# Kernel optimization log

Hardware: AMD Instinct MI355X
Metric: run time of the kernel (lower is better)

The kernel has to match this reference:

```python
import jax, jax.numpy as jnp
import numpy as np

NUM_TAGS = 48
START = 46
STOP = 47
B = 1024
S = 512
NEG_INF = -10000.0


def setup_inputs() -> dict:
    key = jax.random.key(0)
    k1, k2, k3, k4 = jax.random.split(key, 4)
    emissions = jax.random.normal(k1, (B, S, NUM_TAGS), dtype=jnp.float32)
    tags = jax.random.randint(k2, (B, S), 0, 46, dtype=jnp.int32)
    lengths = jax.random.randint(k3, (B,), S // 2, S + 1, dtype=jnp.int32)
    mask = (jnp.arange(S, dtype=jnp.int32)[None, :] < lengths[:, None]).astype(jnp.int32)
    # transitions parameter: uniform(-0.1, 0.1), then constraints from reset_parameters
    transitions = jax.random.uniform(k4, (NUM_TAGS, NUM_TAGS), dtype=jnp.float32,
                                     minval=-0.1, maxval=0.1)
    transitions = transitions.at[:, START].set(NEG_INF).at[STOP, :].set(NEG_INF)
    return {"emissions": emissions, "tags": tags, "mask": mask, "transitions": transitions}


def _log_sum_exp(x, axis):
    # matches torch helper: max + log(clamp(sum(exp(x - max)), 1e-10))
    m = jnp.max(x, axis=axis, keepdims=True)
    s = jnp.sum(jnp.exp(x - m), axis=axis, keepdims=True)
    return jnp.squeeze(m + jnp.log(jnp.clip(s, 1e-10)), axis=axis)


def _forward_alg(emissions, transitions, mask):
    b, s, t = emissions.shape
    alpha0 = jnp.full((b, t), NEG_INF, dtype=emissions.dtype).at[:, START].set(0.0)

    def step(alpha, xs):
        emit, m = xs  # emit: (B, T), m: (B,)
        # (B, prev, next)
        nxt = alpha[:, :, None] + transitions[None, :, :] + emit[:, None, :]
        alpha_t = _log_sum_exp(nxt, axis=1)
        alpha = jnp.where(m[:, None] > 0, alpha_t, alpha)
        return alpha, None

    alpha, _ = jax.lax.scan(step, alpha0,
                            (jnp.transpose(emissions, (1, 0, 2)), mask.T))
    terminal = alpha + transitions[STOP][None, :]
    return _log_sum_exp(terminal, axis=1)  # (B,)


def _score_sequence(emissions, transitions, tags, mask):
    b, s, _ = emissions.shape
    start_col = jnp.full((b, 1), START, dtype=tags.dtype)
    tws = jnp.concatenate([start_col, tags], axis=1)  # (B, S+1)
    # transitions[next, prev] per the original _score_sequence
    trans_sc = transitions[tws[:, 1:], tws[:, :-1]]  # (B, S)
    emit_sc = jnp.take_along_axis(emissions, tags[:, :, None].astype(jnp.int32), axis=2)[..., 0]
    score = jnp.sum((trans_sc + emit_sc) * mask.astype(emissions.dtype), axis=1)
    lengths = jnp.sum(mask, axis=1)
    last_tags = jnp.take_along_axis(tags, (lengths - 1)[:, None], axis=1)[:, 0]
    return score + transitions[STOP, last_tags]


def reference(emissions, tags, mask, transitions):
    log_z = _forward_alg(emissions, transitions, mask)
    gold = _score_sequence(emissions, transitions, tags, mask)
    return jnp.mean(log_z - gold)
```

## Files before the change

kernel.cpp:

```cpp
#include <hip/hip_runtime.h>
#include <hip/hip_bf16.h>
#include <stdint.h>
#include <math.h>

#define SLEN 512
#define NT 48
#define TAG_START 46
#define TAG_STOP 47

typedef __attribute__((ext_vector_type(8))) short bf16x8;
typedef __attribute__((ext_vector_type(4))) float f32x4;

typedef const uint32_t __attribute__((address_space(1)))* gptr_t;
typedef uint32_t __attribute__((address_space(3)))* lptr_t;

__device__ __forceinline__ float bcastf(float v, int l) {
  return __int_as_float(__builtin_amdgcn_readlane(__float_as_int(v), l));
}
__device__ __forceinline__ void gload16(const float* g, float* l) {
  __builtin_amdgcn_global_load_lds((gptr_t)(uintptr_t)g, (lptr_t)(uintptr_t)l,
                                   16, 0, 0);
}
__device__ __forceinline__ uint32_t pk2(float a, float b) {
  float2 f;
  f.x = a;
  f.y = b;
  __hip_bfloat162 bb = __float22bfloat162_rn(f);
  uint32_t u;
  __builtin_memcpy(&u, &bb, 4);
  return u;
}

__global__ __launch_bounds__(64, 1) void crf_fwd_kernel(
    const float* __restrict__ em, const int* __restrict__ tags,
    const int* __restrict__ mask, const float* __restrict__ Tr,
    float* __restrict__ ws) {
  const int b = blockIdx.x;
  const int lane = threadIdx.x;
  const int g = lane >> 4;
  const int n = lane & 15;
  __shared__ __align__(16) float fb[2][32 * NT];
  __shared__ __align__(16) float bbuf[2][32 * NT];

  const int* mrow = mask + (size_t)b * SLEN;
  int lc = 0;
  for (int t = lane; t < SLEN; t += 64) lc += mrow[t];
#pragma unroll
  for (int d = 32; d >= 1; d >>= 1) lc += __shfl_xor(lc, d);
  const int len = lc;

  bf16x8 Af[3][2], Ab[3][2];
#pragma unroll
  for (int t = 0; t < 3; ++t) {
#pragma unroll
    for (int c = 0; c < 2; ++c) {
      union { uint32_t u[4]; bf16x8 v; } tf, tb;
#pragma unroll
      for (int ep = 0; ep < 4; ++ep) {
        float ff[2], fbk[2];
#pragma unroll
        for (int h = 0; h < 2; ++h) {
          const int e = 2 * ep + h;
          const int kl = (e < 4) ? (4 * g + e) : (16 + 4 * g + (e - 4));
          const int ig = 32 * c + kl;
          ff[h] = (ig < NT) ? __expf(Tr[ig * NT + 16 * t + n]) : 0.0f;
          fbk[h] = (ig < NT) ? __expf(Tr[(16 * t + n) * NT + ig]) : 0.0f;
        }
        tf.u[ep] = pk2(ff[0], ff[1]);
        tb.u[ep] = pk2(fbk[0], fbk[1]);
      }
      Af[t][c] = tf.v;
      Ab[t][c] = tb.v;
    }
  }

  f32x4 vf0 = {0.f, 0.f, 0.f, 0.f}, vf1 = vf0, vf2 = vf0;
  if (lane == 48) vf2.z = 1.0f;
  f32x4 vb0 = vf0, vb1 = vf0, vb2 = vf0;
  if (n == 0) {
    const f32x4 one4 = {1.f, 1.f, 1.f, 1.f};
    vb0 = one4;
    vb1 = one4;
    vb2 = one4;
  }
  int cbits = 0;

  const float* embase = em + (size_t)b * SLEN * NT;
  const f32x4 z4 = {0.f, 0.f, 0.f, 0.f};

  auto pairstep = [&](const float* xfp, const float* xbp) {
    const f32x4 xf0 = *(const f32x4*)(xfp + 4 * g);
    const f32x4 xf1 = *(const f32x4*)(xfp + 16 + 4 * g);
    const f32x4 xf2 = *(const f32x4*)(xfp + 32 + 4 * g);
    const f32x4 xb0 = *(const f32x4*)(xbp + 4 * g);
    const f32x4 xb1 = *(const f32x4*)(xbp + 16 + 4 * g);
    const f32x4 xb2 = *(const f32x4*)(xbp + 32 + 4 * g);
    union { uint32_t u[4]; bf16x8 v; } F0, F1;
    F0.u[0] = pk2(vf0.x, vf0.y);
    F0.u[1] = pk2(vf0.z, vf0.w);
    F0.u[2] = pk2(vf1.x, vf1.y);
    F0.u[3] = pk2(vf1.z, vf1.w);
    F1.u[0] = pk2(vf2.x, vf2.y);
    F1.u[1] = pk2(vf2.z, vf2.w);
    F1.u[2] = 0u;
    F1.u[3] = 0u;
    f32x4 af0 = __builtin_amdgcn_mfma_f32_16x16x32_bf16(Af[0][0], F0.v, z4, 0, 0, 0);
    f32x4 af1 = __builtin_amdgcn_mfma_f32_16x16x32_bf16(Af[1][0], F0.v, z4, 0, 0, 0);
    f32x4 af2 = __builtin_amdgcn_mfma_f32_16x16x32_bf16(Af[2][0], F0.v, z4, 0, 0, 0);
    af0 = __builtin_amdgcn_mfma_f32_16x16x32_bf16(Af[0][1], F1.v, af0, 0, 0, 0);
    af1 = __builtin_amdgcn_mfma_f32_16x16x32_bf16(Af[1][1], F1.v, af1, 0, 0, 0);
    af2 = __builtin_amdgcn_mfma_f32_16x16x32_bf16(Af[2][1], F1.v, af2, 0, 0, 0);
    const f32x4 y0 = vb0 * xb0, y1 = vb1 * xb1, y2 = vb2 * xb2;
    union { uint32_t u[4]; bf16x8 v; } G0, G1;
    G0.u[0] = pk2(y0.x, y0.y);
    G0.u[1] = pk2(y0.z, y0.w);
    G0.u[2] = pk2(y1.x, y1.y);
    G0.u[3] = pk2(y1.z, y1.w);
    G1.u[0] = pk2(y2.x, y2.y);
    G1.u[1] = pk2(y2.z, y2.w);
    G1.u[2] = 0u;
    G1.u[3] = 0u;
    f32x4 ab0 = __builtin_amdgcn_mfma_f32_16x16x32_bf16(Ab[0][0], G0.v, z4, 0, 0, 0);
    f32x4 ab1 = __builtin_amdgcn_mfma_f32_16x16x32_bf16(Ab[1][0], G0.v, z4, 0, 0, 0);
    f32x4 ab2 = __builtin_amdgcn_mfma_f32_16x16x32_bf16(Ab[2][0], G0.v, z4, 0, 0, 0);
    ab0 = __builtin_amdgcn_mfma_f32_16x16x32_bf16(Ab[0][1], G1.v, ab0, 0, 0, 0);
    ab1 = __builtin_amdgcn_mfma_f32_16x16x32_bf16(Ab[1][1], G1.v, ab1, 0, 0, 0);
    ab2 = __builtin_amdgcn_mfma_f32_16x16x32_bf16(Ab[2][1], G1.v, ab2, 0, 0, 0);
    vf0 = af0 * xf0;
    vf1 = af1 * xf1;
    vf2 = af2 * xf2;
    vb0 = ab0;
    vb1 = ab1;
    vb2 = ab2;
  };

  auto renorm2 = [&]() {
    f32x4 m4 = __builtin_elementwise_max(__builtin_elementwise_max(vf0, vf1), vf2);
    float mf = fmaxf(fmaxf(m4.x, m4.y), fmaxf(m4.z, fmaxf(m4.w, 1e-30f)));
    mf = fmaxf(fmaxf(bcastf(mf, 0), bcastf(mf, 16)),
               fmaxf(bcastf(mf, 32), bcastf(mf, 48)));
    const int ef = ((__float_as_int(mf) >> 23) & 255) - 126;
    const float sf = __int_as_float((127 - ef) << 23);
    vf0 *= sf;
    vf1 *= sf;
    vf2 *= sf;
    f32x4 n4 = __builtin_elementwise_max(__builtin_elementwise_max(vb0, vb1), vb2);
    float mb = fmaxf(fmaxf(n4.x, n4.y), fmaxf(n4.z, fmaxf(n4.w, 1e-30f)));
    mb = fmaxf(fmaxf(bcastf(mb, 0), bcastf(mb, 16)),
               fmaxf(bcastf(mb, 32), bcastf(mb, 48)));
    const int eb = ((__float_as_int(mb) >> 23) & 255) - 126;
    const float sb = __int_as_float((127 - eb) << 23);
    vb0 *= sb;
    vb1 *= sb;
    vb2 *= sb;
    cbits += ef + eb;
  };

  const int m = len >> 1;
  const int nwin = (m + 31) >> 5;

#pragma unroll
  for (int k = 0; k < 6; ++k) {
    gload16(embase + k * 256 + lane * 4, &fb[0][k * 256]);
    gload16(embase + (size_t)(len - 32) * NT + k * 256 + lane * 4,
            &bbuf[0][k * 256]);
  }

  for (int c = 0; c < nwin; ++c) {
    asm volatile("s_waitcnt vmcnt(0)" ::: "memory");
    if (c + 1 < nwin) {
      const float* fsrc = embase + (size_t)(32 * (c + 1)) * NT;
      const float* bsrc = embase + (size_t)(len - 32 - 32 * (c + 1)) * NT;
#pragma unroll
      for (int k = 0; k < 6; ++k) {
        gload16(fsrc + k * 256 + lane * 4, &fb[(c + 1) & 1][k * 256]);
        gload16(bsrc + k * 256 + lane * 4, &bbuf[(c + 1) & 1][k * 256]);
      }
    }
    float* F = fb[c & 1];
    float* Bw = bbuf[c & 1];
#pragma unroll
    for (int r = 0; r < 6; ++r) {
      f32x4* p = (f32x4*)(F + r * 256 + lane * 4);
      f32x4 vx = *p;
      vx.x = __expf(vx.x);
      vx.y = __expf(vx.y);
      vx.z = __expf(vx.z);
      vx.w = __expf(vx.w);
      *p = vx;
      f32x4* p2 = (f32x4*)(Bw + r * 256 + lane * 4);
      f32x4 vy = *p2;
      vy.x = __expf(vy.x);
      vy.y = __expf(vy.y);
      vy.z = __expf(vy.z);
      vy.w = __expf(vy.w);
      *p2 = vy;
    }
    const int pairs = (m - 32 * c < 32) ? (m - 32 * c) : 32;
    if (pairs == 32) {
      for (int uu = 0; uu < 4; ++uu) {
#pragma unroll
        for (int u = 0; u < 8; ++u) {
          const int s = 8 * uu + u;
          pairstep(F + s * NT, Bw + (31 - s) * NT);
        }
        renorm2();
      }
    } else {
      for (int u = 0; u < pairs; ++u) {
        pairstep(F + u * NT, Bw + (31 - u) * NT);
        if ((u & 7) == 7) renorm2();
      }
      renorm2();
    }
  }

  if (len & 1) {
    const float* rp = embase + (size_t)m * NT;
    f32x4 xb0 = *(const f32x4*)(rp + 4 * g);
    f32x4 xb1 = *(const f32x4*)(rp + 16 + 4 * g);
    f32x4 xb2 = *(const f32x4*)(rp + 32 + 4 * g);
#define EXP4(v) \
  v.x = __expf(v.x); v.y = __expf(v.y); v.z = __expf(v.z); v.w = __expf(v.w)
    EXP4(xb0);
    EXP4(xb1);
    EXP4(xb2);
#undef EXP4
    const f32x4 y0 = vb0 * xb0, y1 = vb1 * xb1, y2 = vb2 * xb2;
    union { uint32_t u[4]; bf16x8 v; } G0, G1;
    G0.u[0] = pk2(y0.x, y0.y);
    G0.u[1] = pk2(y0.z, y0.w);
    G0.u[2] = pk2(y1.x, y1.y);
    G0.u[3] = pk2(y1.z, y1.w);
    G1.u[0] = pk2(y2.x, y2.y);
    G1.u[1] = pk2(y2.z, y2.w);
    G1.u[2] = 0u;
    G1.u[3] = 0u;
    f32x4 ab0 = __builtin_amdgcn_mfma_f32_16x16x32_bf16(Ab[0][0], G0.v, z4, 0, 0, 0);
    f32x4 ab1 = __builtin_amdgcn_mfma_f32_16x16x32_bf16(Ab[1][0], G0.v, z4, 0, 0, 0);
    f32x4 ab2 = __builtin_amdgcn_mfma_f32_16x16x32_bf16(Ab[2][0], G0.v, z4, 0, 0, 0);
    ab0 = __builtin_amdgcn_mfma_f32_16x16x32_bf16(Ab[0][1], G1.v, ab0, 0, 0, 0);
    ab1 = __builtin_amdgcn_mfma_f32_16x16x32_bf16(Ab[1][1], G1.v, ab1, 0, 0, 0);
    ab2 = __builtin_amdgcn_mfma_f32_16x16x32_bf16(Ab[2][1], G1.v, ab2, 0, 0, 0);
    vb0 = ab0;
    vb1 = ab1;
    vb2 = ab2;
  }

  renorm2();
  f32x4 dv = vf0 * vb0 + vf1 * vb1 + vf2 * vb2;
  float dsum = (dv.x + dv.y) + (dv.z + dv.w);
#pragma unroll
  for (int d = 32; d >= 1; d >>= 1) dsum += __shfl_xor(dsum, d);
  const float logZ =
      __logf(dsum) + (float)cbits * 0.69314718055994531f + Tr[TAG_STOP * NT];

  const int* trow = tags + (size_t)b * SLEN;
  float gsc = 0.f;
  for (int t = lane; t < len; t += 64) {
    const int tag = trow[t];
    const int prev = (t == 0) ? TAG_START : trow[t - 1];
    gsc += Tr[tag * NT + prev] + embase[(size_t)t * NT + tag];
  }
#pragma unroll
  for (int d = 32; d >= 1; d >>= 1) gsc += __shfl_xor(gsc, d);

  if (lane == 0) {
    const int last = trow[len - 1];
    ws[b] = logZ - (gsc + Tr[TAG_STOP * NT + last]);
  }
}

__global__ void crf_reduce_kernel(const float* __restrict__ ws,
                                  float* __restrict__ out, int n) {
  const int tid = threadIdx.x;
  float v = (tid < n) ? ws[tid] : 0.f;
#pragma unroll
  for (int d = 32; d >= 1; d >>= 1) v += __shfl_xor(v, d);
  __shared__ float part[16];
  if ((tid & 63) == 0) part[tid >> 6] = v;
  __syncthreads();
  if (tid == 0) {
    float s = 0.f;
    for (int i = 0; i < 16; ++i) s += part[i];
    out[0] = s / (float)n;
  }
}

extern "C" void kernel_launch(void* const* d_in, const int* in_sizes, int n_in,
                              void* d_out, int out_size, void* d_ws, size_t ws_size,
                              hipStream_t stream) {
  const float* em = (const float*)d_in[0];
  const int* tags = (const int*)d_in[1];
  const int* mask = (const int*)d_in[2];
  const float* Tr = (const float*)d_in[3];
  const int B = in_sizes[0] / (SLEN * NT);

  float* ws = (float*)d_ws;
  crf_fwd_kernel<<<B, 64, 0, stream>>>(em, tags, mask, Tr, ws);
  crf_reduce_kernel<<<1, 1024, 0, stream>>>(ws, (float*)d_out, B);
}
```

Measured before the change: 105.2 us.

## Restructure forward/backward recurrence to shorten dependency chain and fold renorm into step

Reorders the per-step recurrence so the elementwise emission multiply happens before the MFMA rather than after, initialising the forward state directly from the START transition row. Renormalisation is folded into the step and done separately on the forward and backward vectors just before packing, instead of as a separate pass after the pair step. The backward emission loads are moved after the forward MFMAs so they can overlap. It also drops the minimum-blocks hint from launch_bounds. This changes where rounding and scaling happen, which could slightly affect accuracy.

```diff
diff --git a/kernel.cpp b/kernel.cpp
--- a/kernel.cpp
+++ b/kernel.cpp
@@ -31,7 +31,23 @@
   return u;
 }
 
-__global__ __launch_bounds__(64, 1) void crf_fwd_kernel(
+#define RENORM3(r0, r1, r2)                                                  \
+  {                                                                          \
+    f32x4 m4_ = __builtin_elementwise_max(                                   \
+        __builtin_elementwise_max(r0, r1), r2);                              \
+    float mx_ = fmaxf(fmaxf(m4_.x, m4_.y), fmaxf(m4_.z, fmaxf(m4_.w,        \
+                                                              1e-30f)));     \
+    mx_ = fmaxf(fmaxf(bcastf(mx_, 0), bcastf(mx_, 16)),                      \
+                fmaxf(bcastf(mx_, 32), bcastf(mx_, 48)));                    \
+    const int ex_ = ((__float_as_int(mx_) >> 23) & 255) - 126;               \
+    const float sc_ = __int_as_float((127 - ex_) << 23);                     \
+    r0 *= sc_;                                                               \
+    r1 *= sc_;                                                               \
+    r2 *= sc_;                                                               \
+    cbits += ex_;                                                            \
+  }
+
+__global__ __launch_bounds__(64) void crf_fwd_kernel(
     const float* __restrict__ em, const int* __restrict__ tags,
     const int* __restrict__ mask, const float* __restrict__ Tr,
     float* __restrict__ ws) {
@@ -39,7 +55,7 @@
   const int lane = threadIdx.x;
   const int g = lane >> 4;
   const int n = lane & 15;
-  __shared__ __align__(16) float fb[2][32 * NT];
+  __shared__ __align__(16) float fbuf[2][32 * NT];
   __shared__ __align__(16) float bbuf[2][32 * NT];
 
   const int* mrow = mask + (size_t)b * SLEN;
@@ -74,27 +90,44 @@
     }
   }
 
-  f32x4 vf0 = {0.f, 0.f, 0.f, 0.f}, vf1 = vf0, vf2 = vf0;
-  if (lane == 48) vf2.z = 1.0f;
-  f32x4 vb0 = vf0, vb1 = vf0, vb2 = vf0;
+  const f32x4 z4 = {0.f, 0.f, 0.f, 0.f};
+  int cbits = 0;
+
+  f32x4 aA0 = z4, aA1 = z4, aA2 = z4;
+  if (n == 0) {
+#define INITA(dst, t)                                             \
+  {                                                               \
+    f32x4 r_;                                                     \
+    r_.x = __expf(Tr[TAG_START * NT + 16 * (t) + 4 * g + 0]);     \
+    r_.y = __expf(Tr[TAG_START * NT + 16 * (t) + 4 * g + 1]);     \
+    r_.z = __expf(Tr[TAG_START * NT + 16 * (t) + 4 * g + 2]);     \
+    r_.w = __expf(Tr[TAG_START * NT + 16 * (t) + 4 * g + 3]);     \
+    dst = r_;                                                     \
+  }
+    INITA(aA0, 0)
+    INITA(aA1, 1)
+    INITA(aA2, 2)
+#undef INITA
+  }
+  f32x4 aB0 = z4, aB1 = z4, aB2 = z4;
   if (n == 0) {
     const f32x4 one4 = {1.f, 1.f, 1.f, 1.f};
-    vb0 = one4;
-    vb1 = one4;
-    vb2 = one4;
-  }
-  int cbits = 0;
-
+    aB0 = one4;
+    aB1 = one4;
+    aB2 = one4;
+  }
+
+  f32x4 vf0 = z4, vf1 = z4, vf2 = z4;
   const float* embase = em + (size_t)b * SLEN * NT;
-  const f32x4 z4 = {0.f, 0.f, 0.f, 0.f};
-
-  auto pairstep = [&](const float* xfp, const float* xbp) {
+
+  auto pairbody = [&](const float* xfp, const float* xbp, bool rn) {
     const f32x4 xf0 = *(const f32x4*)(xfp + 4 * g);
     const f32x4 xf1 = *(const f32x4*)(xfp + 16 + 4 * g);
     const f32x4 xf2 = *(const f32x4*)(xfp + 32 + 4 * g);
-    const f32x4 xb0 = *(const f32x4*)(xbp + 4 * g);
-    const f32x4 xb1 = *(const f32x4*)(xbp + 16 + 4 * g);
-    const f32x4 xb2 = *(const f32x4*)(xbp + 32 + 4 * g);
+    vf0 = aA0 * xf0;
+    vf1 = aA1 * xf1;
+    vf2 = aA2 * xf2;
+    if (rn) RENORM3(vf0, vf1, vf2);
     union { uint32_t u[4]; bf16x8 v; } F0, F1;
     F0.u[0] = pk2(vf0.x, vf0.y);
     F0.u[1] = pk2(vf0.z, vf0.w);
@@ -104,13 +137,19 @@
     F1.u[1] = pk2(vf2.z, vf2.w);
     F1.u[2] = 0u;
     F1.u[3] = 0u;
-    f32x4 af0 = __builtin_amdgcn_mfma_f32_16x16x32_bf16(Af[0][0], F0.v, z4, 0, 0, 0);
-    f32x4 af1 = __builtin_amdgcn_mfma_f32_16x16x32_bf16(Af[1][0], F0.v, z4, 0, 0, 0);
-    f32x4 af2 = __builtin_amdgcn_mfma_f32_16x16x32_bf16(Af[2][0], F0.v, z4, 0, 0, 0);
-    af0 = __builtin_amdgcn_mfma_f32_16x16x32_bf16(Af[0][1], F1.v, af0, 0, 0, 0);
-    af1 = __builtin_amdgcn_mfma_f32_16x16x32_bf16(Af[1][1], F1.v, af1, 0, 0, 0);
-    af2 = __builtin_amdgcn_mfma_f32_16x16x32_bf16(Af[2][1], F1.v, af2, 0, 0, 0);
-    const f32x4 y0 = vb0 * xb0, y1 = vb1 * xb1, y2 = vb2 * xb2;
+    aA0 = __builtin_amdgcn_mfma_f32_16x16x32_bf16(Af[0][0], F0.v, z4, 0, 0, 0);
+    aA1 = __builtin_amdgcn_mfma_f32_16x16x32_bf16(Af[1][0], F0.v, z4, 0, 0, 0);
+    aA2 = __builtin_amdgcn_mfma_f32_16x16x32_bf16(Af[2][0], F0.v, z4, 0, 0, 0);
+    aA0 = __builtin_amdgcn_mfma_f32_16x16x32_bf16(Af[0][1], F1.v, aA0, 0, 0, 0);
+    aA1 = __builtin_amdgcn_mfma_f32_16x16x32_bf16(Af[1][1], F1.v, aA1, 0, 0, 0);
+    aA2 = __builtin_amdgcn_mfma_f32_16x16x32_bf16(Af[2][1], F1.v, aA2, 0, 0, 0);
+    const f32x4 xb0 = *(const f32x4*)(xbp + 4 * g);
+    const f32x4 xb1 = *(const f32x4*)(xbp + 16 + 4 * g);
+    const f32x4 xb2 = *(const f32x4*)(xbp + 32 + 4 * g);
+    f32x4 y0 = aB0 * xb0;
+    f32x4 y1 = aB1 * xb1;
+    f32x4 y2 = aB2 * xb2;
+    if (rn) RENORM3(y0, y1, y2);
     union { uint32_t u[4]; bf16x8 v; } G0, G1;
     G0.u[0] = pk2(y0.x, y0.y);
     G0.u[1] = pk2(y0.z, y0.w);
@@ -120,40 +159,12 @@
     G1.u[1] = pk2(y2.z, y2.w);
     G1.u[2] = 0u;
     G1.u[3] = 0u;
-    f32x4 ab0 = __builtin_amdgcn_mfma_f32_16x16x32_bf16(Ab[0][0], G0.v, z4, 0, 0, 0);
-    f32x4 ab1 = __builtin_amdgcn_mfma_f32_16x16x32_bf16(Ab[1][0], G0.v, z4, 0, 0, 0);
-    f32x4 ab2 = __builtin_amdgcn_mfma_f32_16x16x32_bf16(Ab[2][0], G0.v, z4, 0, 0, 0);
-    ab0 = __builtin_amdgcn_mfma_f32_16x16x32_bf16(Ab[0][1], G1.v, ab0, 0, 0, 0);
-    ab1 = __builtin_amdgcn_mfma_f32_16x16x32_bf16(Ab[1][1], G1.v, ab1, 0, 0, 0);
-    ab2 = __builtin_amdgcn_mfma_f32_16x16x32_bf16(Ab[2][1], G1.v, ab2, 0, 0, 0);
-    vf0 = af0 * xf0;
-    vf1 = af1 * xf1;
-    vf2 = af2 * xf2;
-    vb0 = ab0;
-    vb1 = ab1;
-    vb2 = ab2;
-  };
-
-  auto renorm2 = [&]() {
-    f32x4 m4 = __builtin_elementwise_max(__builtin_elementwise_max(vf0, vf1), vf2);
-    float mf = fmaxf(fmaxf(m4.x, m4.y), fmaxf(m4.z, fmaxf(m4.w, 1e-30f)));
-    mf = fmaxf(fmaxf(bcastf(mf, 0), bcastf(mf, 16)),
-               fmaxf(bcastf(mf, 32), bcastf(mf, 48)));
-    const int ef = ((__float_as_int(mf) >> 23) & 255) - 126;
-    const float sf = __int_as_float((127 - ef) << 23);
-    vf0 *= sf;
-    vf1 *= sf;
-    vf2 *= sf;
-    f32x4 n4 = __builtin_elementwise_max(__builtin_elementwise_max(vb0, vb1), vb2);
-    float mb = fmaxf(fmaxf(n4.x, n4.y), fmaxf(n4.z, fmaxf(n4.w, 1e-30f)));
-    mb = fmaxf(fmaxf(bcastf(mb, 0), bcastf(mb, 16)),
-               fmaxf(bcastf(mb, 32), bcastf(mb, 48)));
-    const int eb = ((__float_as_int(mb) >> 23) & 255) - 126;
-    const float sb = __int_as_float((127 - eb) << 23);
-    vb0 *= sb;
-    vb1 *= sb;
-    vb2 *= sb;
-    cbits += ef + eb;
+    aB0 = __builtin_amdgcn_mfma_f32_16x16x32_bf16(Ab[0][0], G0.v, z4, 0, 0, 0);
+    aB1 = __builtin_amdgcn_mfma_f32_16x16x32_bf16(Ab[1][0], G0.v, z4, 0, 0, 0);
+    aB2 = __builtin_amdgcn_mfma_f32_16x16x32_bf16(Ab[2][0], G0.v, z4, 0, 0, 0);
+    aB0 = __builtin_amdgcn_mfma_f32_16x16x32_bf16(Ab[0][1], G1.v, aB0, 0, 0, 0);
+    aB1 = __builtin_amdgcn_mfma_f32_16x16x32_bf16(Ab[1][1], G1.v, aB1, 0, 0, 0);
+    aB2 = __builtin_amdgcn_mfma_f32_16x16x32_bf16(Ab[2][1], G1.v, aB2, 0, 0, 0);
   };
 
   const int m = len >> 1;
@@ -161,7 +172,7 @@
 
 #pragma unroll
   for (int k = 0; k < 6; ++k) {
-    gload16(embase + k * 256 + lane * 4, &fb[0][k * 256]);
+    gload16(embase + k * 256 + lane * 4, &fbuf[0][k * 256]);
     gload16(embase + (size_t)(len - 32) * NT + k * 256 + lane * 4,
             &bbuf[0][k * 256]);
   }
@@ -173,11 +184,11 @@
       const float* bsrc = embase + (size_t)(len - 32 - 32 * (c + 1)) * NT;
 #pragma unroll
       for (int k = 0; k < 6; ++k) {
-        gload16(fsrc + k * 256 + lane * 4, &fb[(c + 1) & 1][k * 256]);
+        gload16(fsrc + k * 256 + lane * 4, &fbuf[(c + 1) & 1][k * 256]);
         gload16(bsrc + k * 256 + lane * 4, &bbuf[(c + 1) & 1][k * 256]);
       }
     }
-    float* F = fb[c & 1];
+    float* F = fbuf[c & 1];
     float* Bw = bbuf[c & 1];
 #pragma unroll
     for (int r = 0; r < 6; ++r) {
@@ -202,16 +213,13 @@
 #pragma unroll
         for (int u = 0; u < 8; ++u) {
           const int s = 8 * uu + u;
-          pairstep(F + s * NT, Bw + (31 - s) * NT);
+          pairbody(F + s * NT, Bw + (31 - s) * NT, u == 7);
         }
-        renorm2();
       }
     } else {
-      for (int u = 0; u < pairs; ++u) {
-        pairstep(F + u * NT, Bw + (31 - u) * NT);
-        if ((u & 7) == 7) renorm2();
-      }
-      renorm2();
+      for (int u = 0; u < pairs; ++u)
+        pairbody(F + u * NT, Bw + (31 - u) * NT,
+                 ((u & 7) == 7) || (u == pairs - 1));
     }
   }
 
@@ -226,7 +234,7 @@
     EXP4(xb1);
     EXP4(xb2);
 #undef EXP4
-    const f32x4 y0 = vb0 * xb0, y1 = vb1 * xb1, y2 = vb2 * xb2;
+    const f32x4 y0 = aB0 * xb0, y1 = aB1 * xb1, y2 = aB2 * xb2;
     union { uint32_t u[4]; bf16x8 v; } G0, G1;
     G0.u[0] = pk2(y0.x, y0.y);
     G0.u[1] = pk2(y0.z, y0.w);
@@ -236,19 +244,15 @@
     G1.u[1] = pk2(y2.z, y2.w);
     G1.u[2] = 0u;
     G1.u[3] = 0u;
-    f32x4 ab0 = __builtin_amdgcn_mfma_f32_16x16x32_bf16(Ab[0][0], G0.v, z4, 0, 0, 0);
-    f32x4 ab1 = __builtin_amdgcn_mfma_f32_16x16x32_bf16(Ab[1][0], G0.v, z4, 0, 0, 0);
-    f32x4 ab2 = __builtin_amdgcn_mfma_f32_16x16x32_bf16(Ab[2][0], G0.v, z4, 0, 0, 0);
-    ab0 = __builtin_amdgcn_mfma_f32_16x16x32_bf16(Ab[0][1], G1.v, ab0, 0, 0, 0);
-    ab1 = __builtin_amdgcn_mfma_f32_16x16x32_bf16(Ab[1][1], G1.v, ab1, 0, 0, 0);
-    ab2 = __builtin_amdgcn_mfma_f32_16x16x32_bf16(Ab[2][1], G1.v, ab2, 0, 0, 0);
-    vb0 = ab0;
-    vb1 = ab1;
-    vb2 = ab2;
-  }
-
-  renorm2();
-  f32x4 dv = vf0 * vb0 + vf1 * vb1 + vf2 * vb2;
+    aB0 = __builtin_amdgcn_mfma_f32_16x16x32_bf16(Ab[0][0], G0.v, z4, 0, 0, 0);
+    aB1 = __builtin_amdgcn_mfma_f32_16x16x32_bf16(Ab[1][0], G0.v, z4, 0, 0, 0);
+    aB2 = __builtin_amdgcn_mfma_f32_16x16x32_bf16(Ab[2][0], G0.v, z4, 0, 0, 0);
+    aB0 = __builtin_amdgcn_mfma_f32_16x16x32_bf16(Ab[0][1], G1.v, aB0, 0, 0, 0);
+    aB1 = __builtin_amdgcn_mfma_f32_16x16x32_bf16(Ab[1][1], G1.v, aB1, 0, 0, 0);
+    aB2 = __builtin_amdgcn_mfma_f32_16x16x32_bf16(Ab[2][1], G1.v, aB2, 0, 0, 0);
+  }
+
+  f32x4 dv = vf0 * aB0 + vf1 * aB1 + vf2 * aB2;
   float dsum = (dv.x + dv.y) + (dv.z + dv.w);
 #pragma unroll
   for (int d = 32; d >= 1; d >>= 1) dsum += __shfl_xor(dsum, d);
@@ -271,10 +275,10 @@
   }
 }
 
-__global__ void crf_reduce_kernel(const float* __restrict__ ws,
+__global__ void crf_reduce_kernel(const float* __restrict__ wsrc,
                                   float* __restrict__ out, int n) {
   const int tid = threadIdx.x;
-  float v = (tid < n) ? ws[tid] : 0.f;
+  float v = (tid < n) ? wsrc[tid] : 0.f;
 #pragma unroll
   for (int d = 32; d >= 1; d >>= 1) v += __shfl_xor(v, d);
   __shared__ float part[16];
```

Result: faster. 92.47 us (-12.1%).
